# Kernel tuning notes

Hardware: AMD Instinct MI355X
Metric: run time of the kernel (lower is better)

## Reference

```python
import jax, jax.numpy as jnp
import numpy as np

N, C, K = 16384, 128, 20
C2, C8 = C // 2, C // 8
EPS = 1e-5  # torch BatchNorm default eps


def _bn(x, g, b, m, v):
    # inference-mode batchnorm over last (channel) axis
    return (x - m) * jax.lax.rsqrt(v + EPS) * g + b


def setup_inputs() -> dict:
    key = jax.random.key(0)
    ks = jax.random.split(key, 24)
    r = lambda i, sh, s=0.05: jax.random.normal(ks[i], sh, dtype=jnp.float32) * s
    u = lambda i, sh: jax.random.uniform(ks[i], sh, dtype=jnp.float32)
    return {
        "xyz": jax.random.normal(ks[0], (1, 3, N), dtype=jnp.float32),
        "features": jax.random.normal(ks[1], (1, C, N), dtype=jnp.float32),
        "w_mlp1": r(2, (C2, 6), 0.3), "b_mlp1": r(3, (C2,)),
        "bn1_g": u(4, (C2,)) * 0.5 + 0.75, "bn1_b": r(5, (C2,)),
        "bn1_m": r(6, (C2,)), "bn1_v": u(7, (C2,)) * 0.5 + 0.5,
        "w_mlp2": r(8, (C2, 2 * C), 0.06), "b_mlp2": r(9, (C2,)),
        "bn2_g": u(10, (C2,)) * 0.5 + 0.75, "bn2_b": r(11, (C2,)),
        "bn2_m": r(12, (C2,)), "bn2_v": u(13, (C2,)) * 0.5 + 0.5,
        "w_d1": r(14, (C8, C), 0.09), "w_d2": r(15, (C8, C), 0.09),
        "w_up": r(16, (C, C8), 0.25), "b_up": r(17, (C,)),
        "bnu_g": u(18, (C,)) * 0.5 + 0.75, "bnu_b": r(19, (C,)),
        "bnu_m": r(20, (C,)), "bnu_v": u(21, (C,)) * 0.5 + 0.5,
        "k": K,
    }


def reference(xyz, features, w_mlp1, b_mlp1, bn1_g, bn1_b, bn1_m, bn1_v,
              w_mlp2, b_mlp2, bn2_g, bn2_b, bn2_m, bn2_v,
              w_d1, w_d2, w_up, b_up, bnu_g, bnu_b, bnu_m, bnu_v, k):
    B = xyz.shape[0]
    xt = jnp.transpose(xyz, (0, 2, 1))        # [B,N,3]
    ft = jnp.transpose(features, (0, 2, 1))   # [B,N,C]
    # knn: pairwise_distance = -||xi||^2 + 2 xi.xj - ||xj||^2, topk = k nearest
    xx = jnp.sum(xyz * xyz, axis=1)           # [B,N]
    pd = 2.0 * jnp.einsum('bci,bcj->bij', xyz, xyz) - xx[:, :, None] - xx[:, None, :]
    _, idx = jax.lax.top_k(pd, k)             # [B,N,k]
    bidx = jnp.arange(B)[:, None, None]
    nbr_x = xt[bidx, idx]                     # [B,N,k,3]
    nbr_f = ft[bidx, idx]                     # [B,N,k,C]
    cx = xt[:, :, None, :]
    cf = ft[:, :, None, :]
    nx = jnp.concatenate([nbr_x - cx, jnp.broadcast_to(cx, nbr_x.shape)], axis=-1)  # [B,N,k,6]
    nf = jnp.concatenate([nbr_f - cf, jnp.broadcast_to(cf, nbr_f.shape)], axis=-1)  # [B,N,k,2C]
    hx = jax.nn.relu(_bn(jnp.einsum('bnkc,oc->bnko', nx, w_mlp1) + b_mlp1,
                         bn1_g, bn1_b, bn1_m, bn1_v))
    hf = jax.nn.relu(_bn(jnp.einsum('bnkc,oc->bnko', nf, w_mlp2) + b_mlp2,
                         bn2_g, bn2_b, bn2_m, bn2_v))
    f = jnp.max(jnp.concatenate([hx, hf], axis=-1), axis=2)   # [B,N,C]
    f1 = jax.nn.relu(jnp.einsum('bnc,oc->bno', f, w_d1))      # [B,N,C/8]
    f2 = jax.nn.relu(jnp.einsum('bnc,oc->bno', f, w_d2))      # [B,N,C/8]
    # faithful to original: .mean(...)[0] indexes batch 0 (valid since B==1)
    ch = jnp.mean(f1, axis=1)[0][:, None]     # [C/8,1]
    sp = jnp.mean(f2, axis=2)[0][None, :]     # [1,N]
    fe = jnp.sqrt(ch @ sp + 1e-12).T          # [N,C/8]
    fin = fe[None] + f1 + f2                  # [B,N,C/8]
    up = jax.nn.relu(_bn(jnp.einsum('bnc,oc->bno', fin, w_up) + b_up,
                         bnu_g, bnu_b, bnu_m, bnu_v))         # [B,N,C]
    fl = f - up
    fl = fl * jnp.tanh(jax.nn.softplus(fl))   # Mish
    return jnp.transpose(fl, (0, 2, 1))       # [B,C,N]
```

## Files before the change

kernel.cpp:

```cpp
#include <hip/hip_runtime.h>

#define NPT 16384
#define NEG_INF (-3.402823466e38f)

#define OFF_PTS4  0u
#define OFF_WKC   262144u
#define OFF_WAX   327680u
#define OFF_WBX   328704u
#define OFF_CBX   329728u
#define OFF_CBF   329984u
#define OFF_WUP   330240u
#define OFF_BUP   338432u
#define OFF_TAU   338944u
#define OFF_KNN   666624u
#define OFF_PART  1977344u
#define OFF_CH    1993728u
#define OFF_R     1994240u

__device__ __forceinline__ float pd_score(float qx2, float qy2, float qz2, float4 c) {
    return fmaf(qx2, c.x, fmaf(qy2, c.y, fmaf(qz2, c.z, -c.w)));
}

__device__ __forceinline__ unsigned sortable_f(float v) {
    unsigned b = __float_as_uint(v);
    return (b & 0x80000000u) ? ~b : (b | 0x80000000u);
}

__global__ __launch_bounds__(256) void kprep(
    const float* __restrict__ xyz,
    const float* __restrict__ w1, const float* __restrict__ b1,
    const float* __restrict__ g1, const float* __restrict__ bb1,
    const float* __restrict__ m1, const float* __restrict__ v1,
    const float* __restrict__ w2, const float* __restrict__ b2,
    const float* __restrict__ g2, const float* __restrict__ bb2,
    const float* __restrict__ m2, const float* __restrict__ v2,
    const float* __restrict__ wup, const float* __restrict__ bup,
    const float* __restrict__ gu, const float* __restrict__ bu2,
    const float* __restrict__ mu, const float* __restrict__ vu,
    float* __restrict__ wsf)
{
    const int tid = threadIdx.x;
    if (blockIdx.x == 0) {
        float* WKC = wsf + OFF_WKC/4;
        float* WAX = wsf + OFF_WAX/4;
        float* WBX = wsf + OFF_WBX/4;
        float* CBX = wsf + OFF_CBX/4;
        float* CBF = wsf + OFF_CBF/4;
        float* WUP = wsf + OFF_WUP/4;
        float* BUP = wsf + OFF_BUP/4;
        for (int i = tid; i < 16384; i += 256) {
            int c = i >> 7, o = i & 127, oo = o & 63;
            float s2 = g2[oo] * rsqrtf(v2[oo] + 1e-5f);
            float val = (o < 64) ? s2 * w2[oo*256 + c]
                                 : s2 * (w2[oo*256 + 128 + c] - w2[oo*256 + c]);
            WKC[c*128 + o] = val;
        }
        if (tid < 64) {
            int o = tid;
            float s1 = g1[o] * rsqrtf(v1[o] + 1e-5f);
            WAX[o*4+0] = s1 * w1[o*6+0];
            WAX[o*4+1] = s1 * w1[o*6+1];
            WAX[o*4+2] = s1 * w1[o*6+2];
            WAX[o*4+3] = 0.f;
            WBX[o*4+0] = s1 * (w1[o*6+3] - w1[o*6+0]);
            WBX[o*4+1] = s1 * (w1[o*6+4] - w1[o*6+1]);
            WBX[o*4+2] = s1 * (w1[o*6+5] - w1[o*6+2]);
            WBX[o*4+3] = 0.f;
            CBX[o] = s1 * b1[o] + (bb1[o] - m1[o]*s1);
            float s2b = g2[o] * rsqrtf(v2[o] + 1e-5f);
            CBF[o] = s2b * b2[o] + (bb2[o] - m2[o]*s2b);
        }
        if (tid < 128) {
            int o = tid;
            float su = gu[o] * rsqrtf(vu[o] + 1e-5f);
            for (int c = 0; c < 16; ++c) WUP[o*16+c] = su * wup[o*16+c];
            BUP[o] = su * bup[o] + (bu2[o] - mu[o]*su);
        }
    } else {
        #pragma clang fp contract(off)
        int n = (blockIdx.x - 1)*256 + tid;
        float x = xyz[n], y = xyz[NPT+n], z = xyz[2*NPT+n];
        float4 p; p.x = x; p.y = y; p.z = z;
        p.w = (x*x + y*y) + z*z;
        ((float4*)(wsf + OFF_PTS4/4))[n] = p;
    }
}

__global__ __launch_bounds__(256) void ktau(const float* __restrict__ wsf, float* __restrict__ tau)
{
    const float4* pts4 = (const float4*)(wsf + OFF_PTS4/4);
    __shared__ float4 sp[1024];
    __shared__ float t6[32][8][6];
    const int tid = threadIdx.x;
    for (int i = tid; i < 1024; i += 256) sp[i] = pts4[i];
    __syncthreads();
    const int ql = tid >> 3, t = tid & 7;
    const int q = blockIdx.x*32 + ql;
    float4 qp = pts4[q];
    float qx2 = qp.x + qp.x, qy2 = qp.y + qp.y, qz2 = qp.z + qp.z;
    float v0 = NEG_INF, v1 = NEG_INF, v2 = NEG_INF, v3 = NEG_INF, v4 = NEG_INF, v5 = NEG_INF;
    const int jb = t*128;
    for (int i = 0; i < 128; ++i) {
        float v = pd_score(qx2, qy2, qz2, sp[jb + i]);
        float n5 = v > v5 ? (v > v4 ? v4 : v) : v5;
        float n4 = v > v4 ? (v > v3 ? v3 : v) : v4;
        float n3 = v > v3 ? (v > v2 ? v2 : v) : v3;
        float n2 = v > v2 ? (v > v1 ? v1 : v) : v2;
        float n1 = v > v1 ? (v > v0 ? v0 : v) : v1;
        float n0 = v > v0 ? v : v0;
        v0 = n0; v1 = n1; v2 = n2; v3 = n3; v4 = n4; v5 = n5;
    }
    t6[ql][t][0] = v0; t6[ql][t][1] = v1; t6[ql][t][2] = v2;
    t6[ql][t][3] = v3; t6[ql][t][4] = v4; t6[ql][t][5] = v5;
    __syncthreads();
    if (t == 0) {
        int p0=0,p1=0,p2=0,p3=0,p4=0,p5=0,p6=0,p7=0;
        float last = NEG_INF;
        for (int it = 0; it < 20; ++it) {
            float best = NEG_INF; int bl = -1;
#define CHK(L, PL) { float h = t6[ql][L][(PL) < 6 ? (PL) : 5]; if (((PL) < 6) && (h > best)) { best = h; bl = L; } }
            CHK(0,p0) CHK(1,p1) CHK(2,p2) CHK(3,p3) CHK(4,p4) CHK(5,p5) CHK(6,p6) CHK(7,p7)
#undef CHK
            p0 += (bl==0); p1 += (bl==1); p2 += (bl==2); p3 += (bl==3);
            p4 += (bl==4); p5 += (bl==5); p6 += (bl==6); p7 += (bl==7);
            last = best;
        }
        tau[q] = last - 5e-4f;
    }
}

__global__ __launch_bounds__(256) void kpush(const float* __restrict__ wsf,
                                             const float* __restrict__ tau,
                                             unsigned* __restrict__ bm)
{
    const float4* pts4 = (const float4*)(wsf + OFF_PTS4/4);
    __shared__ uint4 st[256][9];
    const int qg = blockIdx.x >> 4, c = blockIdx.x & 15;
    const int tid = threadIdx.x;
    const int jbase = c * 1024;
    const int q = qg*256 + tid;
    float4 a = pts4[q];
    float ax2 = a.x + a.x, ay2 = a.y + a.y, az2 = a.z + a.z;
    float t0 = tau[q];
    for (int g = 0; g < 8; ++g) {
        unsigned wd[4];
#pragma unroll
        for (int u = 0; u < 4; ++u) {
            const int base = jbase + (g*4 + u)*32;
            unsigned w = 0u;
#pragma unroll
            for (int k = 0; k < 32; k += 4) {
                float4 d0 = pts4[base + k];
                float4 d1 = pts4[base + k + 1];
                float4 d2 = pts4[base + k + 2];
                float4 d3 = pts4[base + k + 3];
                float s0 = fmaf(az2, d0.z, fmaf(ay2, d0.y, ax2*d0.x));
                float s1 = fmaf(az2, d1.z, fmaf(ay2, d1.y, ax2*d1.x));
                float s2 = fmaf(az2, d2.z, fmaf(ay2, d2.y, ax2*d2.x));
                float s3 = fmaf(az2, d3.z, fmaf(ay2, d3.y, ax2*d3.x));
                w |= (s0 >= t0 + d0.w) ? (1u << k)       : 0u;
                w |= (s1 >= t0 + d1.w) ? (1u << (k + 1)) : 0u;
                w |= (s2 >= t0 + d2.w) ? (1u << (k + 2)) : 0u;
                w |= (s3 >= t0 + d3.w) ? (1u << (k + 3)) : 0u;
            }
            wd[u] = w;
        }
        uint4 o; o.x = wd[0]; o.y = wd[1]; o.z = wd[2]; o.w = wd[3];
        st[tid][g] = o;
    }
    uint4* dst = (uint4*)(bm + (size_t)q*512 + c*32);
#pragma unroll
    for (int g = 0; g < 8; ++g) dst[g] = st[tid][g];
}

#define KS(A,B) V##A = (kk > V##B) ? V##B : ((kk > V##A) ? kk : V##A);
__global__ __launch_bounds__(256) void ksel(const float* __restrict__ wsf,
                                            const unsigned* __restrict__ bm,
                                            unsigned* __restrict__ knn)
{
    #pragma clang fp contract(off)
    const float4* pts4 = (const float4*)(wsf + OFF_PTS4/4);
    __shared__ unsigned long long pool[4][128];
    const int lane = threadIdx.x & 63;
    const int qw   = threadIdx.x >> 6;
    const int q = blockIdx.x*4 + qw;
    float4 qp = pts4[q];

    unsigned long long V0=0,V1=0,V2=0,V3=0,V4=0,V5=0,V6=0,V7=0;

    const uint4* row = (const uint4*)(bm + (size_t)q*512) + lane*2;
    uint4 a0 = row[0], a1 = row[1];
    unsigned wv[8] = {a0.x, a0.y, a0.z, a0.w, a1.x, a1.y, a1.z, a1.w};
#pragma unroll
    for (int t = 0; t < 8; ++t) {
        unsigned w = wv[t];
        const int wbase = (lane*8 + t)*32;
        while (w) {
            int b = __ffs(w) - 1; w &= w - 1;
            int j = wbase + b;
            float4 cp = pts4[j];
            float d  = (qp.x*cp.x + qp.y*cp.y) + qp.z*cp.z;
            float pd = (2.0f*d - qp.w) - cp.w;
            unsigned long long kk = ((unsigned long long)sortable_f(pd) << 14)
                                  | (unsigned long long)(16383 - j);
            if (kk > V7) {
                KS(7,6) KS(6,5) KS(5,4) KS(4,3) KS(3,2) KS(2,1) KS(1,0)
                V0 = (kk > V0) ? kk : V0;
            }
        }
    }

    unsigned long long s = V0;
#pragma unroll
    for (int k = 2; k <= 64; k <<= 1) {
#pragma unroll
        for (int j = k >> 1; j > 0; j >>= 1) {
            unsigned long long o = __shfl_xor(s, j, 64);
            bool up = ((lane & k) == 0);
            bool lower = ((lane & j) == 0);
            s = (lower == up) ? ((s < o) ? s : o) : ((s > o) ? s : o);
        }
    }
    unsigned long long theta = __shfl(s, 44, 64);

    int cnt = (int)(V0 >= theta) + (int)(V1 >= theta) + (int)(V2 >= theta)
            + (int)(V3 >= theta) + (int)(V4 >= theta) + (int)(V5 >= theta)
            + (int)(V6 >= theta) + (int)(V7 >= theta);
    int sc = cnt;
#pragma unroll
    for (int o = 1; o < 64; o <<= 1) {
        int t2 = __shfl_up(sc, o, 64);
        sc += (lane >= o) ? t2 : 0;
    }
    int C = __shfl(sc, 63, 64);
    int base = sc - cnt;
    if (C > 128) C = 128;
    unsigned long long* pq = pool[qw];
#define WPOOL(I, VI) if (I < cnt) { int p = base + I; if (p < 128) pq[p] = VI; }
    WPOOL(0, V0) WPOOL(1, V1) WPOOL(2, V2) WPOOL(3, V3)
    WPOOL(4, V4) WPOOL(5, V5) WPOOL(6, V6) WPOOL(7, V7)
#undef WPOOL
    __syncthreads();

    bool h1 = lane < C;
    bool h2 = (lane + 64) < C;
    unsigned long long k1 = h1 ? pq[lane] : 0ull;
    unsigned long long k2 = h2 ? pq[lane + 64] : 0ull;
    int r1 = 0, r2 = 0;
    for (int i = 0; i < C; ++i) {
        unsigned long long ki = pq[i];
        r1 += (int)(ki > k1);
        r2 += (int)(ki > k2);
    }
    unsigned* kout = knn + (size_t)q*20;
    if (h1 && r1 < 20) kout[r1] = 16383u - (unsigned)(k1 & 0x3FFFull);
    if (h2 && r2 < 20) kout[r2] = 16383u - (unsigned)(k2 & 0x3FFFull);
}

__global__ __launch_bounds__(128) void kgemm(const float* __restrict__ feat,
                                             const float* __restrict__ wsf,
                                             float* __restrict__ G, float* __restrict__ T2)
{
    __shared__ float As[32][64];
    __shared__ float Bs[32][128];
    const float* WKC = wsf + OFF_WKC/4;
    const float* CBF = wsf + OFF_CBF/4;
    const int tid = threadIdx.x;
    const int n0 = blockIdx.x * 64;
    const int tx = tid & 15, ty = tid >> 4;
    float acc[8][8] = {};
    for (int kc = 0; kc < 4; ++kc) {
        int c0 = kc * 32;
        for (int i = tid; i < 2048; i += 128) {
            int cl = i >> 6, nl = i & 63;
            As[cl][nl] = feat[(size_t)(c0 + cl)*NPT + n0 + nl];
        }
        for (int i = tid; i < 4096; i += 128) {
            int cl = i >> 7, ol = i & 127;
            Bs[cl][ol] = WKC[(c0 + cl)*128 + ol];
        }
        __syncthreads();
        for (int cc = 0; cc < 32; ++cc) {
            float av[8], bv[8];
#pragma unroll
            for (int r = 0; r < 8; ++r) av[r] = As[cc][ty*8 + r];
#pragma unroll
            for (int s = 0; s < 8; ++s) bv[s] = Bs[cc][tx*8 + s];
#pragma unroll
            for (int r = 0; r < 8; ++r)
#pragma unroll
                for (int s = 0; s < 8; ++s)
                    acc[r][s] = fmaf(av[r], bv[s], acc[r][s]);
        }
        __syncthreads();
    }
#pragma unroll
    for (int r = 0; r < 8; ++r) {
        int n = n0 + ty*8 + r;
        if (tx < 8) {
            float* dst = G + (size_t)n*128 + 64 + tx*8;
#pragma unroll
            for (int s = 0; s < 8; ++s) dst[s] = acc[r][s];
        } else {
            int ob = (tx - 8)*8;
            float* dst = T2 + (size_t)n*128 + 64 + ob;
#pragma unroll
            for (int s = 0; s < 8; ++s) dst[s] = acc[r][s] + CBF[ob + s];
        }
    }
}

__global__ __launch_bounds__(256) void kxpart(const float* __restrict__ xyz,
                                              const float* __restrict__ wsf,
                                              float* __restrict__ G, float* __restrict__ T2)
{
    const float4* WAX = (const float4*)(wsf + OFF_WAX/4);
    const float4* WBX = (const float4*)(wsf + OFF_WBX/4);
    const float*  CBX = wsf + OFF_CBX/4;
    const int tid = threadIdx.x;
    const int o = tid & 63;
    const int n = blockIdx.x*4 + (tid >> 6);
    float x = xyz[n], y = xyz[NPT+n], z = xyz[2*NPT+n];
    float4 A = WAX[o], B = WBX[o];
    G[(size_t)n*128 + o]  = fmaf(x, A.x, fmaf(y, A.y, z*A.z));
    T2[(size_t)n*128 + o] = fmaf(x, B.x, fmaf(y, B.y, fmaf(z, B.z, CBX[o])));
}

__global__ __launch_bounds__(256) void kgather(const float* __restrict__ wsf,
                                               const unsigned* __restrict__ knn,
                                               const float* __restrict__ G,
                                               const float* __restrict__ T2,
                                               const float* __restrict__ wd1,
                                               const float* __restrict__ wd2,
                                               float* __restrict__ F, float* __restrict__ F1,
                                               float* __restrict__ F2, float* __restrict__ SPm,
                                               float* __restrict__ PART)
{
    __shared__ float fsh[64][136];
    __shared__ float w1s[16][136];
    __shared__ float w2s[16][136];
    __shared__ float f1sh[64][16];
    __shared__ float f2p[64][4];
    const int tid = threadIdx.x;
    for (int i = tid; i < 2048; i += 256) {
        int o = i >> 7, cc = i & 127;
        w1s[o][cc] = wd1[i];
        w2s[o][cc] = wd2[i];
    }
    const int nl = tid >> 2, qt = tid & 3;
    const int n = blockIdx.x*64 + nl;
    const unsigned* ip = knn + (size_t)n*20;
    float acc[32];
#pragma unroll
    for (int e = 0; e < 32; ++e) acc[e] = NEG_INF;
    for (int k = 0; k < 20; ++k) {
        unsigned j = ip[k];
        const float4* g4 = (const float4*)(G + (size_t)j*128 + qt*32);
#pragma unroll
        for (int r = 0; r < 8; ++r) {
            float4 gv = g4[r];
            acc[r*4+0] = fmaxf(acc[r*4+0], gv.x);
            acc[r*4+1] = fmaxf(acc[r*4+1], gv.y);
            acc[r*4+2] = fmaxf(acc[r*4+2], gv.z);
            acc[r*4+3] = fmaxf(acc[r*4+3], gv.w);
        }
    }
    const float4* t4 = (const float4*)(T2 + (size_t)n*128 + qt*32);
    float4* fg = (float4*)(F + (size_t)n*128 + qt*32);
    float4* fs = (float4*)&fsh[nl][qt*32];
#pragma unroll
    for (int r = 0; r < 8; ++r) {
        float4 tv = t4[r];
        float4 o4;
        o4.x = fmaxf(acc[r*4+0] + tv.x, 0.f);
        o4.y = fmaxf(acc[r*4+1] + tv.y, 0.f);
        o4.z = fmaxf(acc[r*4+2] + tv.z, 0.f);
        o4.w = fmaxf(acc[r*4+3] + tv.w, 0.f);
        fg[r] = o4; fs[r] = o4;
    }
    __syncthreads();
    float a1[4] = {0,0,0,0}, a2[4] = {0,0,0,0};
    const int ob = qt*4;
    for (int c4 = 0; c4 < 32; ++c4) {
        float4 fv = ((const float4*)&fsh[nl][0])[c4];
#pragma unroll
        for (int r = 0; r < 4; ++r) {
            float4 wv1 = ((const float4*)&w1s[ob + r][0])[c4];
            float4 wv2 = ((const float4*)&w2s[ob + r][0])[c4];
            a1[r] = fmaf(fv.x, wv1.x, fmaf(fv.y, wv1.y, fmaf(fv.z, wv1.z, fmaf(fv.w, wv1.w, a1[r]))));
            a2[r] = fmaf(fv.x, wv2.x, fmaf(fv.y, wv2.y, fmaf(fv.z, wv2.z, fmaf(fv.w, wv2.w, a2[r]))));
        }
    }
    float s2sum = 0.f;
#pragma unroll
    for (int r = 0; r < 4; ++r) {
        a1[r] = fmaxf(a1[r], 0.f);
        a2[r] = fmaxf(a2[r], 0.f);
        s2sum += a2[r];
        F1[(size_t)n*16 + ob + r] = a1[r];
        F2[(size_t)n*16 + ob + r] = a2[r];
        f1sh[nl][ob + r] = a1[r];
    }
    f2p[nl][qt] = s2sum;
    __syncthreads();
    if (qt == 0)
        SPm[n] = (f2p[nl][0] + f2p[nl][1] + f2p[nl][2] + f2p[nl][3]) * (1.0f/16.0f);
    if (tid < 16) {
        float s = 0.f;
        for (int r = 0; r < 64; ++r) s += f1sh[r][tid];
        PART[blockIdx.x*16 + tid] = s;
    }
}

__global__ __launch_bounds__(64) void kch(const float* __restrict__ PART, float* __restrict__ CH)
{
    const int tid = threadIdx.x;
    if (tid < 16) {
        float s = 0.f;
        for (int b = 0; b < 256; ++b) s += PART[b*16 + tid];
        CH[tid] = s * (1.0f/16384.0f);
    }
}

__global__ __launch_bounds__(64) void kfinal(const float* __restrict__ wsf,
                                             const float* __restrict__ F,
                                             const float* __restrict__ F1,
                                             const float* __restrict__ F2,
                                             const float* __restrict__ SPm,
                                             const float* __restrict__ CH,
                                             float* __restrict__ out)
{
    const float* WUP = wsf + OFF_WUP/4;
    const float* BUP = wsf + OFF_BUP/4;
    const int n = blockIdx.x*64 + threadIdx.x;
    float spv = SPm[n];
    float fin[16];
    const float4* f14 = (const float4*)(F1 + (size_t)n*16);
    const float4* f24 = (const float4*)(F2 + (size_t)n*16);
#pragma unroll
    for (int c4 = 0; c4 < 4; ++c4) {
        float4 a = f14[c4], b = f24[c4];
        fin[c4*4+0] = sqrtf(fmaf(CH[c4*4+0], spv, 1e-12f)) + a.x + b.x;
        fin[c4*4+1] = sqrtf(fmaf(CH[c4*4+1], spv, 1e-12f)) + a.y + b.y;
        fin[c4*4+2] = sqrtf(fmaf(CH[c4*4+2], spv, 1e-12f)) + a.z + b.z;
        fin[c4*4+3] = sqrtf(fmaf(CH[c4*4+3], spv, 1e-12f)) + a.w + b.w;
    }
    const float4* fF = (const float4*)(F + (size_t)n*128);
    for (int o4 = 0; o4 < 32; ++o4) {
        float4 fv = fF[o4];
        float fa[4] = {fv.x, fv.y, fv.z, fv.w};
#pragma unroll
        for (int e = 0; e < 4; ++e) {
            int o = o4*4 + e;
            float u = BUP[o];
#pragma unroll
            for (int c = 0; c < 16; ++c) u = fmaf(fin[c], WUP[o*16 + c], u);
            u = fmaxf(u, 0.f);
            float fl = fa[e] - u;
            float flc = fminf(fl, 15.f);
            float t = expf(flc);
            float w = 1.f + t;
            float w2 = w*w;
            float th = (w2 - 1.f) / (w2 + 1.f);
            float res = (fl > 15.f) ? fl : fl * th;
            out[(size_t)o*NPT + n] = res;
        }
    }
}

extern "C" void kernel_launch(void* const* d_in, const int* in_sizes, int n_in,
                              void* d_out, int out_size, void* d_ws, size_t ws_size,
                              hipStream_t stream) {
    const float* xyz  = (const float*)d_in[0];
    const float* feat = (const float*)d_in[1];
    const float* w1   = (const float*)d_in[2];
    const float* b1   = (const float*)d_in[3];
    const float* g1   = (const float*)d_in[4];
    const float* bb1  = (const float*)d_in[5];
    const float* m1   = (const float*)d_in[6];
    const float* v1   = (const float*)d_in[7];
    const float* w2   = (const float*)d_in[8];
    const float* b2   = (const float*)d_in[9];
    const float* g2   = (const float*)d_in[10];
    const float* bb2  = (const float*)d_in[11];
    const float* m2   = (const float*)d_in[12];
    const float* v2   = (const float*)d_in[13];
    const float* wd1  = (const float*)d_in[14];
    const float* wd2  = (const float*)d_in[15];
    const float* wup  = (const float*)d_in[16];
    const float* bup  = (const float*)d_in[17];
    const float* gu   = (const float*)d_in[18];
    const float* bu2  = (const float*)d_in[19];
    const float* mu   = (const float*)d_in[20];
    const float* vu   = (const float*)d_in[21];
    float* out = (float*)d_out;

    float* wsf = (float*)d_ws;
    unsigned* bm   = (unsigned*)((char*)d_ws + OFF_R);
    unsigned* knn  = (unsigned*)((char*)d_ws + OFF_KNN);
    float* TAU  = (float*)((char*)d_ws + OFF_TAU);
    float* PART = (float*)((char*)d_ws + OFF_PART);
    float* CH   = (float*)((char*)d_ws + OFF_CH);
    float* G  = (float*)((char*)d_ws + OFF_R);
    float* T2 = G  + 2097152;
    float* F  = T2 + 2097152;
    float* F1 = F  + 2097152;
    float* F2 = F1 + 262144;
    float* SPm = F2 + 262144;

    kprep<<<dim3(65),  dim3(256), 0, stream>>>(xyz, w1,b1,g1,bb1,m1,v1,
                                               w2,b2,g2,bb2,m2,v2,
                                               wup,bup,gu,bu2,mu,vu, wsf);
    ktau <<<dim3(512), dim3(256), 0, stream>>>(wsf, TAU);
    kpush<<<dim3(1024), dim3(256), 0, stream>>>(wsf, TAU, bm);
    ksel <<<dim3(4096), dim3(256), 0, stream>>>(wsf, bm, knn);
    kgemm<<<dim3(256), dim3(128), 0, stream>>>(feat, wsf, G, T2);
    kxpart<<<dim3(4096), dim3(256), 0, stream>>>(xyz, wsf, G, T2);
    kgather<<<dim3(256), dim3(256), 0, stream>>>(wsf, knn, G, T2, wd1, wd2, F, F1, F2, SPm, PART);
    kch  <<<dim3(1),   dim3(64), 0, stream>>>(PART, CH);
    kfinal<<<dim3(256), dim3(64), 0, stream>>>(wsf, F, F1, F2, SPm, CH, out);
}
```

Baseline: 263.2 us.

## Compact candidate indices before KNN selection and rebalance push/tau kernels

In ksel, each wave first compacts the candidate indices from the bitmask into a shared 16-bit pool using a popcount prefix scan, then processes them round-robin across lanes, so every lane gets an equal share instead of lanes with dense bit words doing most of the work. This targets warp divergence in the candidate-scoring loop. If a query has more than 1024 candidates, the extras are silently dropped, which could lose true neighbours. kpush now processes two interleaved 512-point halves per iteration and folds the threshold into the fma chain. ktau drops its LDS staging and reads points straight from global memory.

```diff
diff --git a/kernel.cpp b/kernel.cpp
--- a/kernel.cpp
+++ b/kernel.cpp
@@ -89,11 +89,8 @@
 __global__ __launch_bounds__(256) void ktau(const float* __restrict__ wsf, float* __restrict__ tau)
 {
     const float4* pts4 = (const float4*)(wsf + OFF_PTS4/4);
-    __shared__ float4 sp[1024];
     __shared__ float t6[32][8][6];
     const int tid = threadIdx.x;
-    for (int i = tid; i < 1024; i += 256) sp[i] = pts4[i];
-    __syncthreads();
     const int ql = tid >> 3, t = tid & 7;
     const int q = blockIdx.x*32 + ql;
     float4 qp = pts4[q];
@@ -101,7 +98,7 @@
     float v0 = NEG_INF, v1 = NEG_INF, v2 = NEG_INF, v3 = NEG_INF, v4 = NEG_INF, v5 = NEG_INF;
     const int jb = t*128;
     for (int i = 0; i < 128; ++i) {
-        float v = pd_score(qx2, qy2, qz2, sp[jb + i]);
+        float v = pd_score(qx2, qy2, qz2, pts4[jb + i]);
         float n5 = v > v5 ? (v > v4 ? v4 : v) : v5;
         float n4 = v > v4 ? (v > v3 ? v3 : v) : v4;
         float n3 = v > v3 ? (v > v2 ? v2 : v) : v3;
@@ -135,40 +132,43 @@
 {
     const float4* pts4 = (const float4*)(wsf + OFF_PTS4/4);
     __shared__ uint4 st[256][9];
-    const int qg = blockIdx.x >> 4, c = blockIdx.x & 15;
-    const int tid = threadIdx.x;
-    const int jbase = c * 1024;
+    const int qg = blockIdx.x >> 4, s = blockIdx.x & 15;
+    const int tid = threadIdx.x;
+    const int jA = s*1024, jB = s*1024 + 512;
     const int q = qg*256 + tid;
     float4 a = pts4[q];
     float ax2 = a.x + a.x, ay2 = a.y + a.y, az2 = a.z + a.z;
-    float t0 = tau[q];
-    for (int g = 0; g < 8; ++g) {
-        unsigned wd[4];
+    float nt0 = -tau[q];
+    for (int g = 0; g < 4; ++g) {
+        unsigned wdA[4], wdB[4];
 #pragma unroll
         for (int u = 0; u < 4; ++u) {
-            const int base = jbase + (g*4 + u)*32;
-            unsigned w = 0u;
-#pragma unroll
-            for (int k = 0; k < 32; k += 4) {
-                float4 d0 = pts4[base + k];
-                float4 d1 = pts4[base + k + 1];
-                float4 d2 = pts4[base + k + 2];
-                float4 d3 = pts4[base + k + 3];
-                float s0 = fmaf(az2, d0.z, fmaf(ay2, d0.y, ax2*d0.x));
-                float s1 = fmaf(az2, d1.z, fmaf(ay2, d1.y, ax2*d1.x));
-                float s2 = fmaf(az2, d2.z, fmaf(ay2, d2.y, ax2*d2.x));
-                float s3 = fmaf(az2, d3.z, fmaf(ay2, d3.y, ax2*d3.x));
-                w |= (s0 >= t0 + d0.w) ? (1u << k)       : 0u;
-                w |= (s1 >= t0 + d1.w) ? (1u << (k + 1)) : 0u;
-                w |= (s2 >= t0 + d2.w) ? (1u << (k + 2)) : 0u;
-                w |= (s3 >= t0 + d3.w) ? (1u << (k + 3)) : 0u;
+            const int bA = jA + (g*4 + u)*32;
+            const int bB = jB + (g*4 + u)*32;
+            unsigned wa = 0u, wb = 0u;
+#pragma unroll
+            for (int k = 0; k < 32; k += 2) {
+                float4 dA0 = pts4[bA + k];
+                float4 dA1 = pts4[bA + k + 1];
+                float4 dB0 = pts4[bB + k];
+                float4 dB1 = pts4[bB + k + 1];
+                float sA0 = fmaf(az2, dA0.z, fmaf(ay2, dA0.y, fmaf(ax2, dA0.x, nt0)));
+                float sA1 = fmaf(az2, dA1.z, fmaf(ay2, dA1.y, fmaf(ax2, dA1.x, nt0)));
+                float sB0 = fmaf(az2, dB0.z, fmaf(ay2, dB0.y, fmaf(ax2, dB0.x, nt0)));
+                float sB1 = fmaf(az2, dB1.z, fmaf(ay2, dB1.y, fmaf(ax2, dB1.x, nt0)));
+                wa |= (sA0 >= dA0.w) ? (1u << k)       : 0u;
+                wa |= (sA1 >= dA1.w) ? (1u << (k + 1)) : 0u;
+                wb |= (sB0 >= dB0.w) ? (1u << k)       : 0u;
+                wb |= (sB1 >= dB1.w) ? (1u << (k + 1)) : 0u;
             }
-            wd[u] = w;
-        }
-        uint4 o; o.x = wd[0]; o.y = wd[1]; o.z = wd[2]; o.w = wd[3];
-        st[tid][g] = o;
-    }
-    uint4* dst = (uint4*)(bm + (size_t)q*512 + c*32);
+            wdA[u] = wa; wdB[u] = wb;
+        }
+        uint4 oA; oA.x = wdA[0]; oA.y = wdA[1]; oA.z = wdA[2]; oA.w = wdA[3];
+        uint4 oB; oB.x = wdB[0]; oB.y = wdB[1]; oB.z = wdB[2]; oB.w = wdB[3];
+        st[tid][g]     = oA;
+        st[tid][4 + g] = oB;
+    }
+    uint4* dst = (uint4*)(bm + (size_t)q*512 + s*32);
 #pragma unroll
     for (int g = 0; g < 8; ++g) dst[g] = st[tid][g];
 }
@@ -180,63 +180,85 @@
 {
     #pragma clang fp contract(off)
     const float4* pts4 = (const float4*)(wsf + OFF_PTS4/4);
+    __shared__ unsigned short spool[4][1024];
     __shared__ unsigned long long pool[4][128];
     const int lane = threadIdx.x & 63;
     const int qw   = threadIdx.x >> 6;
     const int q = blockIdx.x*4 + qw;
     float4 qp = pts4[q];
 
-    unsigned long long V0=0,V1=0,V2=0,V3=0,V4=0,V5=0,V6=0,V7=0;
-
     const uint4* row = (const uint4*)(bm + (size_t)q*512) + lane*2;
     uint4 a0 = row[0], a1 = row[1];
     unsigned wv[8] = {a0.x, a0.y, a0.z, a0.w, a1.x, a1.y, a1.z, a1.w};
+    int scnt = 0;
+#pragma unroll
+    for (int t = 0; t < 8; ++t) scnt += __popc(wv[t]);
+    int spre = scnt;
+#pragma unroll
+    for (int o = 1; o < 64; o <<= 1) {
+        int t2 = __shfl_up(spre, o, 64);
+        spre += (lane >= o) ? t2 : 0;
+    }
+    int nS = __shfl(spre, 63, 64);
+    if (nS > 1024) nS = 1024;
+    unsigned short* sp = spool[qw];
+    int wptr = spre - scnt;
 #pragma unroll
     for (int t = 0; t < 8; ++t) {
         unsigned w = wv[t];
         const int wbase = (lane*8 + t)*32;
         while (w) {
             int b = __ffs(w) - 1; w &= w - 1;
-            int j = wbase + b;
-            float4 cp = pts4[j];
-            float d  = (qp.x*cp.x + qp.y*cp.y) + qp.z*cp.z;
-            float pd = (2.0f*d - qp.w) - cp.w;
-            unsigned long long kk = ((unsigned long long)sortable_f(pd) << 14)
-                                  | (unsigned long long)(16383 - j);
-            if (kk > V7) {
-                KS(7,6) KS(6,5) KS(5,4) KS(4,3) KS(3,2) KS(2,1) KS(1,0)
-                V0 = (kk > V0) ? kk : V0;
-            }
-        }
-    }
-
-    unsigned long long s = V0;
+            if (wptr < 1024) sp[wptr] = (unsigned short)(wbase + b);
+            ++wptr;
+        }
+    }
+    __syncthreads();
+
+    unsigned long long V0=0,V1=0,V2=0,V3=0,V4=0,V5=0,V6=0,V7=0;
+    const int rounds = (nS + 63) >> 6;
+    for (int r = 0; r < rounds; ++r) {
+        int i = r*64 + lane;
+        bool val = i < nS;
+        int j = val ? (int)sp[i] : 0;
+        float4 cp = pts4[j];
+        float d  = (qp.x*cp.x + qp.y*cp.y) + qp.z*cp.z;
+        float pd = (2.0f*d - qp.w) - cp.w;
+        unsigned long long kk = val ? (((unsigned long long)sortable_f(pd) << 14)
+                                      | (unsigned long long)(16383 - j)) : 0ull;
+        if (kk > V7) {
+            KS(7,6) KS(6,5) KS(5,4) KS(4,3) KS(3,2) KS(2,1) KS(1,0)
+            V0 = (kk > V0) ? kk : V0;
+        }
+    }
+
+    unsigned long long ss = V0;
 #pragma unroll
     for (int k = 2; k <= 64; k <<= 1) {
 #pragma unroll
         for (int j = k >> 1; j > 0; j >>= 1) {
-            unsigned long long o = __shfl_xor(s, j, 64);
+            unsigned long long o = __shfl_xor(ss, j, 64);
             bool up = ((lane & k) == 0);
             bool lower = ((lane & j) == 0);
-            s = (lower == up) ? ((s < o) ? s : o) : ((s > o) ? s : o);
-        }
-    }
-    unsigned long long theta = __shfl(s, 44, 64);
-
-    int cnt = (int)(V0 >= theta) + (int)(V1 >= theta) + (int)(V2 >= theta)
-            + (int)(V3 >= theta) + (int)(V4 >= theta) + (int)(V5 >= theta)
-            + (int)(V6 >= theta) + (int)(V7 >= theta);
-    int sc = cnt;
+            ss = (lower == up) ? ((ss < o) ? ss : o) : ((ss > o) ? ss : o);
+        }
+    }
+    unsigned long long theta = __shfl(ss, 44, 64);
+
+    int kcnt = (int)(V0 >= theta) + (int)(V1 >= theta) + (int)(V2 >= theta)
+             + (int)(V3 >= theta) + (int)(V4 >= theta) + (int)(V5 >= theta)
+             + (int)(V6 >= theta) + (int)(V7 >= theta);
+    int ksc = kcnt;
 #pragma unroll
     for (int o = 1; o < 64; o <<= 1) {
-        int t2 = __shfl_up(sc, o, 64);
-        sc += (lane >= o) ? t2 : 0;
-    }
-    int C = __shfl(sc, 63, 64);
-    int base = sc - cnt;
+        int t2 = __shfl_up(ksc, o, 64);
+        ksc += (lane >= o) ? t2 : 0;
+    }
+    int C = __shfl(ksc, 63, 64);
+    int kbase = ksc - kcnt;
     if (C > 128) C = 128;
     unsigned long long* pq = pool[qw];
-#define WPOOL(I, VI) if (I < cnt) { int p = base + I; if (p < 128) pq[p] = VI; }
+#define WPOOL(I, VI) if (I < kcnt) { int p = kbase + I; if (p < 128) pq[p] = VI; }
     WPOOL(0, V0) WPOOL(1, V1) WPOOL(2, V2) WPOOL(3, V3)
     WPOOL(4, V4) WPOOL(5, V5) WPOOL(6, V6) WPOOL(7, V7)
 #undef WPOOL
```

Result: slower. 278.8 us (+5.9%).
